# Kernel tuning notes

Measured on AMD Instinct MI355X. Metric: run time of the kernel, lower is better.

The kernel has to match this reference:

```python
import jax, jax.numpy as jnp
import numpy as np

DIM = 1024
HEADS = 16
SCALE = DIM ** (-0.5)  # NOTE: module scales by full dim, not head_dim


def setup_inputs() -> dict:
    key = jax.random.key(0)
    k1, k2, k3, k4 = jax.random.split(key, 4)
    x = jax.random.normal(k1, (4, 2048, DIM), dtype=jnp.float32)
    # torch Linear weights: y = x @ W.T
    w_qkv = jax.random.normal(k2, (3 * DIM, DIM), dtype=jnp.float32) * (DIM ** -0.5)
    w_out = jax.random.normal(k3, (DIM, DIM), dtype=jnp.float32) * (DIM ** -0.5)
    b_out = jax.random.normal(k4, (DIM,), dtype=jnp.float32) * 0.01
    return {"x": x, "w_qkv": w_qkv, "w_out": w_out, "b_out": b_out}


def reference(x, w_qkv, w_out, b_out):
    b, n, _ = x.shape
    h = HEADS
    d = DIM // h
    qkv = x @ w_qkv.T                                   # [b, n, 3*dim]
    qkv = qkv.reshape(b, n, 3, h, d)                    # split (qkv h d)
    qkv = jnp.transpose(qkv, (2, 0, 3, 1, 4))           # [3, b, h, n, d]
    q, k, v = qkv[0], qkv[1], qkv[2]
    dots = jnp.einsum('bhid,bhjd->bhij', q, k) * SCALE  # [b, h, n, n]
    attn = jax.nn.softmax(dots, axis=-1)
    out = jnp.einsum('bhij,bhjd->bhid', attn, v)        # [b, h, n, d]
    out = jnp.transpose(out, (0, 2, 1, 3)).reshape(b, n, h * d)
    return out @ w_out.T + b_out
```

## Files before the change

kernel.cpp:

```cpp
#include <hip/hip_runtime.h>

typedef short bf16x8 __attribute__((ext_vector_type(8)));
typedef _Float16 f16x8 __attribute__((ext_vector_type(8)));
typedef __fp16 fp16x2 __attribute__((ext_vector_type(2)));
typedef float f32x4 __attribute__((ext_vector_type(4)));
typedef float f32x16 __attribute__((ext_vector_type(16)));
typedef unsigned u32x2 __attribute__((ext_vector_type(2)));

static __device__ __forceinline__ unsigned short f2bf(float f) {
  union { float f; unsigned u; } v; v.f = f;
  unsigned r = v.u + 0x7fffu + ((v.u >> 16) & 1u);
  return (unsigned short)(r >> 16);
}

static __device__ __forceinline__ unsigned short f2h(float f) {
  union { _Float16 h; unsigned short u; } c; c.h = (_Float16)f; return c.u;
}

static __device__ __forceinline__ unsigned pkh(float lo, float hi) {
  union { fp16x2 h; unsigned u; } c;
  c.h = __builtin_amdgcn_cvt_pkrtz(lo, hi);
  return c.u;
}

static __device__ __forceinline__ void gll16(const unsigned short* g,
                                             unsigned short* l) {
  __builtin_amdgcn_global_load_lds(
      (const __attribute__((address_space(1))) unsigned int*)g,
      (__attribute__((address_space(3))) unsigned int*)l, 16, 0, 0);
}

__global__ void cvt3_kernel(const float* __restrict__ a,
                            const float* __restrict__ b,
                            const float* __restrict__ c,
                            unsigned short* __restrict__ dst) {
  int i = blockIdx.x * blockDim.x + threadIdx.x;
  const float* src; int off;
  if (i < 2097152) { src = a; off = 0; }
  else if (i < 2883584) { src = b; off = 2097152; }
  else { src = c; off = 2883584; }
  float4 f = ((const float4*)src)[i - off];
  ushort4 o;
  o.x = f2bf(f.x); o.y = f2bf(f.y); o.z = f2bf(f.z); o.w = f2bf(f.w);
  ((ushort4*)dst)[i] = o;
}

#define TM 128
#define TN 128
#define BK 64

template <int EPI>
__global__ __launch_bounds__(256, 3)
void gemm_bt(const unsigned short* __restrict__ X,
             const unsigned short* __restrict__ W,
             unsigned short* __restrict__ QKV, float* __restrict__ OUT,
             const float* __restrict__ bias, int M, int N, int K) {
  __shared__ __align__(16) unsigned short As[TM * BK];
  __shared__ __align__(16) unsigned short Bs[TN * BK];

  const int tid = threadIdx.x;
  const int lane = tid & 63;
  const int wave = tid >> 6;
  const int quad = lane >> 4;
  const int l16 = lane & 15;
  const int wm = wave >> 1, wn = wave & 1;
  const int rc = l16 & 7;

  const int m0 = blockIdx.y * TM;
  const int n0 = blockIdx.x * TN;

  const int sr = lane >> 3;
  const int gsc = ((lane & 7) ^ sr) * 8;

  f32x4 zero = {0.f, 0.f, 0.f, 0.f};
  f32x4 acc[4][4];
#pragma unroll
  for (int i = 0; i < 4; i++)
#pragma unroll
    for (int j = 0; j < 4; j++) acc[i][j] = zero;

  for (int k0 = 0; k0 < K; k0 += BK) {
    __syncthreads();
#pragma unroll
    for (int c = 0; c < 4; c++) {
      int row = wave * 32 + c * 8;
      gll16(&X[(size_t)(m0 + row + sr) * K + k0 + gsc], &As[row * BK]);
      gll16(&W[(size_t)(n0 + row + sr) * K + k0 + gsc], &Bs[row * BK]);
    }
    __syncthreads();
#pragma unroll
    for (int kk = 0; kk < 2; kk++) {
      bf16x8 af[4], bfr[4];
      const int csw = ((kk * 4 + quad) ^ rc) * 8;
#pragma unroll
      for (int t = 0; t < 4; t++) {
        af[t]  = *(const bf16x8*)&As[(wm * 64 + t * 16 + l16) * BK + csw];
        bfr[t] = *(const bf16x8*)&Bs[(wn * 64 + t * 16 + l16) * BK + csw];
      }
#pragma unroll
      for (int mt = 0; mt < 4; mt++)
#pragma unroll
        for (int nt = 0; nt < 4; nt++)
          acc[mt][nt] = __builtin_amdgcn_mfma_f32_16x16x32_bf16(
              af[mt], bfr[nt], acc[mt][nt], 0, 0, 0);
    }
  }

#pragma unroll
  for (int mt = 0; mt < 4; mt++) {
#pragma unroll
    for (int nt = 0; nt < 4; nt++) {
      if (EPI == 0) {
        int nbase = n0 + wn * 64 + nt * 16;
        int which = nbase >> 10;
        if (which == 2) {
          int rem = (nbase + l16) & 1023;
          int h = rem >> 6, dd = rem & 63;
          int growb = m0 + wm * 64 + mt * 16 + quad * 4;
          int b = growb >> 11, nn0 = growb & 2047;
          ushort4 o;
          o.x = f2h(acc[mt][nt][0]);
          o.y = f2h(acc[mt][nt][1]);
          o.z = f2h(acc[mt][nt][2]);
          o.w = f2h(acc[mt][nt][3]);
          *(ushort4*)&QKV[16777216u + (((size_t)(b * 16 + h) * 64 + dd) << 11) + nn0] = o;
        } else {
#pragma unroll
          for (int r = 0; r < 4; r++) {
            int grow = m0 + wm * 64 + mt * 16 + quad * 4 + r;
            int gcol = nbase + l16;
            int rem = gcol & 1023;
            int h = rem >> 6, dd = rem & 63;
            float v = acc[mt][nt][r];
            if (which == 0) v *= 0.04508422f;
            int b = grow >> 11, nn = grow & 2047;
            QKV[(size_t)which * 8388608 +
                ((size_t)(b * 16 + h) * 2048 + nn) * 64 + dd] = f2bf(v);
          }
        }
      } else {
#pragma unroll
        for (int r = 0; r < 4; r++) {
          int grow = m0 + wm * 64 + mt * 16 + quad * 4 + r;
          int gcol = n0 + wn * 64 + nt * 16 + l16;
          OUT[(size_t)grow * N + gcol] = acc[mt][nt][r] + bias[gcol];
        }
      }
    }
  }
}

#define SK 72

__global__ __launch_bounds__(512, 4)
void attn_kernel(const unsigned short* __restrict__ Qg,
                 const unsigned short* __restrict__ Kg,
                 const unsigned short* __restrict__ Vg,
                 unsigned short* __restrict__ AO) {
  __shared__ __align__(16) unsigned short K_s[2][64 * SK];
  __shared__ __align__(16) unsigned short V_s[2][64 * SK];

  const int tid = threadIdx.x;
  const int lane = tid & 63;
  const int wave = tid >> 6;
  const int l31 = lane & 31;
  const int hh = lane >> 5;

  const int id = blockIdx.x + 8 * blockIdx.y;
  const int xcd = id & 7;
  const int slot = id >> 3;
  const int bh = xcd * 8 + (slot & 7);
  const int qb = slot >> 3;

  const size_t base = (size_t)bh * 131072;
  const int q0 = qb * 256 + wave * 32;

  bf16x8 bq[4];
#pragma unroll
  for (int ks = 0; ks < 4; ks++)
    bq[ks] = *(const bf16x8*)&Qg[base + (size_t)(q0 + l31) * 64 + ks * 16 + hh * 8];

  f32x16 O[2];
#pragma unroll
  for (int dt = 0; dt < 2; dt++)
#pragma unroll
    for (int r = 0; r < 16; r++) O[dt][r] = 0.f;
  float lrow = 0.f;

  const int sr = lane >> 3, sc = (lane & 7) * 8;
  const unsigned short* Kp = Kg + base + (size_t)(wave * 8 + sr) * 64 + sc;
  const unsigned short* Vp = Vg + base + (size_t)(wave * 8 + sr) * 2048 + sc;
  const int woff = (wave * 8 + sr) * SK + sc;

  uint4 kr, vr;
  kr = *(const uint4*)Kp;
  vr = *(const uint4*)Vp;
  *(uint4*)&K_s[0][woff] = kr;
  *(uint4*)&V_s[0][woff] = vr;
  __syncthreads();

  for (int t = 0; t < 32; t++) {
    const unsigned short* Kc = K_s[t & 1];
    const unsigned short* Vc = V_s[t & 1];
    if (t < 31) {
      kr = *(const uint4*)(Kp + (size_t)(t + 1) * 4096);
      vr = *(const uint4*)(Vp + (size_t)(t + 1) * 64);
    }

    f32x16 S[2];
#pragma unroll
    for (int sub = 0; sub < 2; sub++) {
      f32x16 a;
#pragma unroll
      for (int r = 0; r < 16; r++) a[r] = 0.f;
#pragma unroll
      for (int ks = 0; ks < 4; ks++) {
        bf16x8 kf = *(const bf16x8*)&Kc[(sub * 32 + l31) * SK + ks * 16 + hh * 8];
        a = __builtin_amdgcn_mfma_f32_32x32x16_bf16(kf, bq[ks], a, 0, 0, 0);
      }
      S[sub] = a;
    }

    float rsum = 0.f;
#pragma unroll
    for (int sub = 0; sub < 2; sub++)
#pragma unroll
      for (int r = 0; r < 16; r++) {
        float p = __builtin_amdgcn_exp2f(S[sub][r]);
        S[sub][r] = p;
        rsum += p;
      }
    lrow += rsum;

#pragma unroll
    for (int win = 0; win < 4; win++) {
      const int sub = win >> 1, kk = win & 1;
      const int g0 = kk * 2, g1 = kk * 2 + 1;
      unsigned a00 = pkh(S[sub][4 * g0 + 0], S[sub][4 * g0 + 1]);
      unsigned a01 = pkh(S[sub][4 * g0 + 2], S[sub][4 * g0 + 3]);
      unsigned a10 = pkh(S[sub][4 * g1 + 0], S[sub][4 * g1 + 1]);
      unsigned a11 = pkh(S[sub][4 * g1 + 2], S[sub][4 * g1 + 3]);
      union { unsigned u[4]; f16x8 v; } fr;
#if __has_builtin(__builtin_amdgcn_permlane32_swap)
      u32x2 r0 = __builtin_amdgcn_permlane32_swap(a00, a10, false, false);
      u32x2 r1 = __builtin_amdgcn_permlane32_swap(a01, a11, false, false);
      fr.u[0] = r0.x; fr.u[1] = r1.x; fr.u[2] = r0.y; fr.u[3] = r1.y;
#else
      unsigned b00 = __shfl_xor((int)a00, 32);
      unsigned b01 = __shfl_xor((int)a01, 32);
      unsigned b10 = __shfl_xor((int)a10, 32);
      unsigned b11 = __shfl_xor((int)a11, 32);
      fr.u[0] = hh ? b10 : a00;
      fr.u[1] = hh ? b11 : a01;
      fr.u[2] = hh ? a10 : b00;
      fr.u[3] = hh ? a11 : b01;
#endif
      f16x8 pf = fr.v;
#pragma unroll
      for (int dt = 0; dt < 2; dt++) {
        f16x8 vf = *(const f16x8*)&Vc[(dt * 32 + l31) * SK + win * 16 + hh * 8];
        O[dt] = __builtin_amdgcn_mfma_f32_32x32x16_f16(vf, pf, O[dt], 0, 0, 0);
      }
    }

    if (t < 31) {
      const int nb = (t + 1) & 1;
      *(uint4*)&K_s[nb][woff] = kr;
      *(uint4*)&V_s[nb][woff] = vr;
    }
    __syncthreads();
  }

  const int b4 = bh >> 4, head = bh & 15;
  lrow += __shfl_xor(lrow, 32);
  float inv = 1.0f / lrow;
  int row = b4 * 2048 + q0 + l31;
#pragma unroll
  for (int dt = 0; dt < 2; dt++)
#pragma unroll
    for (int g = 0; g < 4; g++) {
      ushort4 o;
      o.x = f2bf(O[dt][4 * g + 0] * inv);
      o.y = f2bf(O[dt][4 * g + 1] * inv);
      o.z = f2bf(O[dt][4 * g + 2] * inv);
      o.w = f2bf(O[dt][4 * g + 3] * inv);
      *(ushort4*)&AO[(size_t)row * 1024 + head * 64 + dt * 32 + 8 * g + 4 * hh] = o;
    }
}

extern "C" void kernel_launch(void* const* d_in, const int* in_sizes, int n_in,
                              void* d_out, int out_size, void* d_ws,
                              size_t ws_size, hipStream_t stream) {
  const float* x     = (const float*)d_in[0];
  const float* w_qkv = (const float*)d_in[1];
  const float* w_out = (const float*)d_in[2];
  const float* b_out = (const float*)d_in[3];
  float* out = (float*)d_out;

  unsigned short* ws = (unsigned short*)d_ws;
  unsigned short* Xbf  = ws;
  unsigned short* Wqkv = ws + 8388608;
  unsigned short* Wout = ws + 11534336;
  unsigned short* QKV  = ws + 12582912;
  unsigned short* AO   = ws;

  cvt3_kernel<<<12288, 256, 0, stream>>>(x, w_qkv, w_out, Xbf);

  gemm_bt<0><<<dim3(3072 / TN, 8192 / TM), 256, 0, stream>>>(
      Xbf, Wqkv, QKV, nullptr, nullptr, 8192, 3072, 1024);

  attn_kernel<<<dim3(8, 64), 512, 0, stream>>>(
      QKV, QKV + 8388608, QKV + 16777216, AO);

  gemm_bt<1><<<dim3(1024 / TN, 8192 / TM), 256, 0, stream>>>(
      AO, Wout, nullptr, out, b_out, 8192, 1024, 1024);
}
```

Baseline: 250.0 us.

## Replace QKV projection GEMM with 256x256-tile, 8-wave pipelined kernel

```diff
diff --git a/kernel.cpp b/kernel.cpp
--- a/kernel.cpp
+++ b/kernel.cpp
@@ -45,15 +45,253 @@
   ((ushort4*)dst)[i] = o;
 }
 
+__global__ __launch_bounds__(512, 2)
+void gemm256_qkv(const unsigned short* __restrict__ X,
+                 const unsigned short* __restrict__ W,
+                 unsigned short* __restrict__ QKV, int M, int N, int K) {
+  __shared__ __align__(16) unsigned short As[2][2][256 * 32];
+  __shared__ __align__(16) unsigned short Bs[2][2][256 * 32];
+
+  const int tid = threadIdx.x;
+  const int lane = tid & 63;
+  const int wave = tid >> 6;
+  const int wm = wave >> 2;
+  const int wn = wave & 3;
+  const int quad = lane >> 4;
+  const int l16 = lane & 15;
+
+  const int id = blockIdx.x + 12 * blockIdx.y;
+  const int nid = (id & 7) * 48 + (id >> 3);
+  const int n0 = (nid % 12) * 256;
+  const int m0 = (nid / 12) * 256;
+
+  const int rl = lane >> 2;
+  const int sl = lane & 3;
+  const int gchunk = ((sl ^ (rl & 3)) * 8);
+  const int aslot = (quad ^ (l16 & 3)) * 8;
+
+  auto stageA = [&](int b, int kh, int T) {
+#pragma unroll
+    for (int c = 0; c < 2; c++) {
+      int row = wave * 32 + c * 16;
+      gll16(&X[(size_t)(m0 + row + rl) * K + T * 64 + kh * 32 + gchunk],
+            &As[b][kh][row * 32]);
+    }
+  };
+  auto stageB = [&](int b, int kh, int T) {
+#pragma unroll
+    for (int c = 0; c < 2; c++) {
+      int row = wave * 32 + c * 16;
+      gll16(&W[(size_t)(n0 + row + rl) * K + T * 64 + kh * 32 + gchunk],
+            &Bs[b][kh][row * 32]);
+    }
+  };
+
+  f32x4 zero = {0.f, 0.f, 0.f, 0.f};
+  f32x4 acc[8][4];
+#pragma unroll
+  for (int i = 0; i < 8; i++)
+#pragma unroll
+    for (int j = 0; j < 4; j++) acc[i][j] = zero;
+
+  bf16x8 af[8], bfb[4];
+
+  const int NI = K >> 7;
+
+  stageA(0, 0, 0); stageB(0, 0, 0); stageA(0, 1, 0); stageB(0, 1, 0);
+  stageA(1, 0, 1); stageB(1, 0, 1);
+  asm volatile("s_waitcnt vmcnt(4)" ::: "memory");
+  __builtin_amdgcn_s_barrier();
+
+  for (int i = 0; i < NI; i++) {
+    const int T = 2 * i;
+    const int U = T + 1;
+    const bool more = (i + 1 < NI);
+
+#pragma unroll
+    for (int mt = 0; mt < 8; mt++)
+      af[mt] = *(const bf16x8*)&As[0][0][(wm * 128 + mt * 16 + l16) * 32 + aslot];
+#pragma unroll
+    for (int nt = 0; nt < 2; nt++)
+      bfb[nt] = *(const bf16x8*)&Bs[0][0][(wn * 64 + nt * 16 + l16) * 32 + aslot];
+    stageA(1, 1, U);
+    __builtin_amdgcn_s_barrier();
+    __builtin_amdgcn_s_setprio(1);
+#pragma unroll
+    for (int mt = 0; mt < 8; mt++)
+#pragma unroll
+      for (int nt = 0; nt < 2; nt++)
+        acc[mt][nt] = __builtin_amdgcn_mfma_f32_16x16x32_bf16(
+            af[mt], bfb[nt], acc[mt][nt], 0, 0, 0);
+    __builtin_amdgcn_s_setprio(0);
+    __builtin_amdgcn_s_barrier();
+
+#pragma unroll
+    for (int nt = 0; nt < 2; nt++)
+      bfb[2 + nt] = *(const bf16x8*)&Bs[0][0][(wn * 64 + (2 + nt) * 16 + l16) * 32 + aslot];
+    stageB(1, 1, U);
+    __builtin_amdgcn_s_barrier();
+    __builtin_amdgcn_s_setprio(1);
+#pragma unroll
+    for (int mt = 0; mt < 8; mt++)
+#pragma unroll
+      for (int nt = 0; nt < 2; nt++)
+        acc[mt][2 + nt] = __builtin_amdgcn_mfma_f32_16x16x32_bf16(
+            af[mt], bfb[2 + nt], acc[mt][2 + nt], 0, 0, 0);
+    __builtin_amdgcn_s_setprio(0);
+    __builtin_amdgcn_s_barrier();
+
+#pragma unroll
+    for (int mt = 0; mt < 8; mt++)
+      af[mt] = *(const bf16x8*)&As[0][1][(wm * 128 + mt * 16 + l16) * 32 + aslot];
+#pragma unroll
+    for (int nt = 0; nt < 2; nt++)
+      bfb[nt] = *(const bf16x8*)&Bs[0][1][(wn * 64 + nt * 16 + l16) * 32 + aslot];
+    if (more) stageA(0, 0, T + 2);
+    __builtin_amdgcn_s_barrier();
+    __builtin_amdgcn_s_setprio(1);
+#pragma unroll
+    for (int mt = 0; mt < 8; mt++)
+#pragma unroll
+      for (int nt = 0; nt < 2; nt++)
+        acc[mt][nt] = __builtin_amdgcn_mfma_f32_16x16x32_bf16(
+            af[mt], bfb[nt], acc[mt][nt], 0, 0, 0);
+    __builtin_amdgcn_s_setprio(0);
+    __builtin_amdgcn_s_barrier();
+
+#pragma unroll
+    for (int nt = 0; nt < 2; nt++)
+      bfb[2 + nt] = *(const bf16x8*)&Bs[0][1][(wn * 64 + (2 + nt) * 16 + l16) * 32 + aslot];
+    if (more) {
+      stageB(0, 0, T + 2);
+      asm volatile("s_waitcnt vmcnt(4)" ::: "memory");
+    } else {
+      asm volatile("s_waitcnt vmcnt(0)" ::: "memory");
+    }
+    __builtin_amdgcn_s_barrier();
+    __builtin_amdgcn_s_setprio(1);
+#pragma unroll
+    for (int mt = 0; mt < 8; mt++)
+#pragma unroll
+      for (int nt = 0; nt < 2; nt++)
+        acc[mt][2 + nt] = __builtin_amdgcn_mfma_f32_16x16x32_bf16(
+            af[mt], bfb[2 + nt], acc[mt][2 + nt], 0, 0, 0);
+    __builtin_amdgcn_s_setprio(0);
+    __builtin_amdgcn_s_barrier();
+
+#pragma unroll
+    for (int mt = 0; mt < 8; mt++)
+      af[mt] = *(const bf16x8*)&As[1][0][(wm * 128 + mt * 16 + l16) * 32 + aslot];
+#pragma unroll
+    for (int nt = 0; nt < 2; nt++)
+      bfb[nt] = *(const bf16x8*)&Bs[1][0][(wn * 64 + nt * 16 + l16) * 32 + aslot];
+    if (more) stageA(0, 1, T + 2);
+    __builtin_amdgcn_s_barrier();
+    __builtin_amdgcn_s_setprio(1);
+#pragma unroll
+    for (int mt = 0; mt < 8; mt++)
+#pragma unroll
+      for (int nt = 0; nt < 2; nt++)
+        acc[mt][nt] = __builtin_amdgcn_mfma_f32_16x16x32_bf16(
+            af[mt], bfb[nt], acc[mt][nt], 0, 0, 0);
+    __builtin_amdgcn_s_setprio(0);
+    __builtin_amdgcn_s_barrier();
+
+#pragma unroll
+    for (int nt = 0; nt < 2; nt++)
+      bfb[2 + nt] = *(const bf16x8*)&Bs[1][0][(wn * 64 + (2 + nt) * 16 + l16) * 32 + aslot];
+    if (more) stageB(0, 1, T + 2);
+    __builtin_amdgcn_s_barrier();
+    __builtin_amdgcn_s_setprio(1);
+#pragma unroll
+    for (int mt = 0; mt < 8; mt++)
+#pragma unroll
+      for (int nt = 0; nt < 2; nt++)
+        acc[mt][2 + nt] = __builtin_amdgcn_mfma_f32_16x16x32_bf16(
+            af[mt], bfb[2 + nt], acc[mt][2 + nt], 0, 0, 0);
+    __builtin_amdgcn_s_setprio(0);
+    __builtin_amdgcn_s_barrier();
+
+#pragma unroll
+    for (int mt = 0; mt < 8; mt++)
+      af[mt] = *(const bf16x8*)&As[1][1][(wm * 128 + mt * 16 + l16) * 32 + aslot];
+#pragma unroll
+    for (int nt = 0; nt < 2; nt++)
+      bfb[nt] = *(const bf16x8*)&Bs[1][1][(wn * 64 + nt * 16 + l16) * 32 + aslot];
+    if (more) stageA(1, 0, U + 2);
+    __builtin_amdgcn_s_barrier();
+    __builtin_amdgcn_s_setprio(1);
+#pragma unroll
+    for (int mt = 0; mt < 8; mt++)
+#pragma unroll
+      for (int nt = 0; nt < 2; nt++)
+        acc[mt][nt] = __builtin_amdgcn_mfma_f32_16x16x32_bf16(
+            af[mt], bfb[nt], acc[mt][nt], 0, 0, 0);
+    __builtin_amdgcn_s_setprio(0);
+    __builtin_amdgcn_s_barrier();
+
+#pragma unroll
+    for (int nt = 0; nt < 2; nt++)
+      bfb[2 + nt] = *(const bf16x8*)&Bs[1][1][(wn * 64 + (2 + nt) * 16 + l16) * 32 + aslot];
+    if (more) {
+      stageB(1, 0, U + 2);
+      asm volatile("s_waitcnt vmcnt(4)" ::: "memory");
+    }
+    __builtin_amdgcn_s_barrier();
+    __builtin_amdgcn_s_setprio(1);
+#pragma unroll
+    for (int mt = 0; mt < 8; mt++)
+#pragma unroll
+      for (int nt = 0; nt < 2; nt++)
+        acc[mt][2 + nt] = __builtin_amdgcn_mfma_f32_16x16x32_bf16(
+            af[mt], bfb[2 + nt], acc[mt][2 + nt], 0, 0, 0);
+    __builtin_amdgcn_s_setprio(0);
+    __builtin_amdgcn_s_barrier();
+  }
+
+#pragma unroll
+  for (int mt = 0; mt < 8; mt++) {
+#pragma unroll
+    for (int nt = 0; nt < 4; nt++) {
+      int nbase = n0 + wn * 64 + nt * 16;
+      int which = nbase >> 10;
+      if (which == 2) {
+        int rem = (nbase + l16) & 1023;
+        int h = rem >> 6, dd = rem & 63;
+        int growb = m0 + wm * 128 + mt * 16 + quad * 4;
+        int b = growb >> 11, nn0 = growb & 2047;
+        ushort4 o;
+        o.x = f2h(acc[mt][nt][0]);
+        o.y = f2h(acc[mt][nt][1]);
+        o.z = f2h(acc[mt][nt][2]);
+        o.w = f2h(acc[mt][nt][3]);
+        *(ushort4*)&QKV[16777216u + (((size_t)(b * 16 + h) * 64 + dd) << 11) + nn0] = o;
+      } else {
+#pragma unroll
+        for (int r = 0; r < 4; r++) {
+          int grow = m0 + wm * 128 + mt * 16 + quad * 4 + r;
+          int gcol = nbase + l16;
+          int rem = gcol & 1023;
+          int h = rem >> 6, dd = rem & 63;
+          float v = acc[mt][nt][r];
+          if (which == 0) v *= 0.04508422f;
+          int b = grow >> 11, nn = grow & 2047;
+          QKV[(size_t)which * 8388608 +
+              ((size_t)(b * 16 + h) * 2048 + nn) * 64 + dd] = f2bf(v);
+        }
+      }
+    }
+  }
+}
+
 #define TM 128
 #define TN 128
 #define BK 64
 
-template <int EPI>
 __global__ __launch_bounds__(256, 3)
 void gemm_bt(const unsigned short* __restrict__ X,
              const unsigned short* __restrict__ W,
-             unsigned short* __restrict__ QKV, float* __restrict__ OUT,
+             float* __restrict__ OUT,
              const float* __restrict__ bias, int M, int N, int K) {
   __shared__ __align__(16) unsigned short As[TM * BK];
   __shared__ __align__(16) unsigned short Bs[TN * BK];
@@ -110,41 +348,11 @@
   for (int mt = 0; mt < 4; mt++) {
 #pragma unroll
     for (int nt = 0; nt < 4; nt++) {
-      if (EPI == 0) {
-        int nbase = n0 + wn * 64 + nt * 16;
-        int which = nbase >> 10;
-        if (which == 2) {
-          int rem = (nbase + l16) & 1023;
-          int h = rem >> 6, dd = rem & 63;
-          int growb = m0 + wm * 64 + mt * 16 + quad * 4;
-          int b = growb >> 11, nn0 = growb & 2047;
-          ushort4 o;
-          o.x = f2h(acc[mt][nt][0]);
-          o.y = f2h(acc[mt][nt][1]);
-          o.z = f2h(acc[mt][nt][2]);
-          o.w = f2h(acc[mt][nt][3]);
-          *(ushort4*)&QKV[16777216u + (((size_t)(b * 16 + h) * 64 + dd) << 11) + nn0] = o;
-        } else {
-#pragma unroll
-          for (int r = 0; r < 4; r++) {
-            int grow = m0 + wm * 64 + mt * 16 + quad * 4 + r;
-            int gcol = nbase + l16;
-            int rem = gcol & 1023;
-            int h = rem >> 6, dd = rem & 63;
-            float v = acc[mt][nt][r];
-            if (which == 0) v *= 0.04508422f;
-            int b = grow >> 11, nn = grow & 2047;
-            QKV[(size_t)which * 8388608 +
-                ((size_t)(b * 16 + h) * 2048 + nn) * 64 + dd] = f2bf(v);
-          }
-        }
-      } else {
-#pragma unroll
-        for (int r = 0; r < 4; r++) {
-          int grow = m0 + wm * 64 + mt * 16 + quad * 4 + r;
-          int gcol = n0 + wn * 64 + nt * 16 + l16;
-          OUT[(size_t)grow * N + gcol] = acc[mt][nt][r] + bias[gcol];
-        }
+#pragma unroll
+      for (int r = 0; r < 4; r++) {
+        int grow = m0 + wm * 64 + mt * 16 + quad * 4 + r;
+        int gcol = n0 + wn * 64 + nt * 16 + l16;
+        OUT[(size_t)grow * N + gcol] = acc[mt][nt][r] + bias[gcol];
       }
     }
   }
@@ -306,12 +514,12 @@
 
   cvt3_kernel<<<12288, 256, 0, stream>>>(x, w_qkv, w_out, Xbf);
 
-  gemm_bt<0><<<dim3(3072 / TN, 8192 / TM), 256, 0, stream>>>(
-      Xbf, Wqkv, QKV, nullptr, nullptr, 8192, 3072, 1024);
+  gemm256_qkv<<<dim3(12, 32), 512, 0, stream>>>(
+      Xbf, Wqkv, QKV, 8192, 3072, 1024);
 
   attn_kernel<<<dim3(8, 64), 512, 0, stream>>>(
       QKV, QKV + 8388608, QKV + 16777216, AO);
 
-  gemm_bt<1><<<dim3(1024 / TN, 8192 / TM), 256, 0, stream>>>(
-      AO, Wout, nullptr, out, b_out, 8192, 1024, 1024);
-}
+  gemm_bt<<<dim3(1024 / TN, 8192 / TM), 256, 0, stream>>>(
+      AO, Wout, out, b_out, 8192, 1024, 1024);
+}
```

After: 267.2 us. +6.9%, slower.

## Replace QKV projection GEMM with 256x256 tiled, software-pipelined 8-wave kernel

Applied to the files above, without the earlier changes.

```diff
diff --git a/kernel.cpp b/kernel.cpp
--- a/kernel.cpp
+++ b/kernel.cpp
@@ -45,15 +45,193 @@
   ((ushort4*)dst)[i] = o;
 }
 
+__global__ __launch_bounds__(512, 2)
+void gemm256_qkv(const unsigned short* __restrict__ X,
+                 const unsigned short* __restrict__ W,
+                 unsigned short* __restrict__ QKV, int M, int N, int K) {
+  __shared__ __align__(16) unsigned short As[2][2][128 * 64];
+  __shared__ __align__(16) unsigned short Bs[2][2][128 * 64];
+
+  const int tid = threadIdx.x;
+  const int lane = tid & 63;
+  const int wave = tid >> 6;
+  const int wm = wave >> 2;
+  const int wn = wave & 3;
+  const int quad = lane >> 4;
+  const int l16 = lane & 15;
+  const int l8 = l16 & 7;
+
+  const int id = blockIdx.x + 12 * blockIdx.y;
+  const int nid = (id & 7) * 48 + (id >> 3);
+  const int n0 = (nid % 12) * 256;
+  const int m0 = (nid / 12) * 256;
+
+  const int sr8 = lane >> 3;
+  const int gsc = ((lane & 7) ^ sr8) * 8;
+
+  auto stA = [&](int b, int mh, int T) {
+#pragma unroll
+    for (int c = 0; c < 2; c++) {
+      int row = wave * 16 + c * 8;
+      gll16(&X[(size_t)(m0 + mh * 128 + row + sr8) * K + T * 64 + gsc],
+            &As[b][mh][row * 64]);
+    }
+  };
+  auto stB = [&](int b, int nh, int T) {
+#pragma unroll
+    for (int c = 0; c < 2; c++) {
+      int row = wave * 16 + c * 8;
+      gll16(&W[(size_t)(n0 + nh * 128 + row + sr8) * K + T * 64 + gsc],
+            &Bs[b][nh][row * 64]);
+    }
+  };
+
+  f32x4 zero = {0.f, 0.f, 0.f, 0.f};
+  f32x4 acc[8][4];
+#pragma unroll
+  for (int i = 0; i < 8; i++)
+#pragma unroll
+    for (int j = 0; j < 4; j++) acc[i][j] = zero;
+
+  bf16x8 af[4][2], bf[2][2];
+
+  auto ldA = [&](int b, int mh) {
+#pragma unroll
+    for (int m = 0; m < 4; m++)
+#pragma unroll
+      for (int kk = 0; kk < 2; kk++)
+        af[m][kk] = *(const bf16x8*)&As[b][mh][(wm * 64 + m * 16 + l16) * 64 +
+                                               ((kk * 4 + quad) ^ l8) * 8];
+  };
+  auto ldB = [&](int b, int nh) {
+#pragma unroll
+    for (int n = 0; n < 2; n++)
+#pragma unroll
+      for (int kk = 0; kk < 2; kk++)
+        bf[n][kk] = *(const bf16x8*)&Bs[b][nh][(wn * 32 + n * 16 + l16) * 64 +
+                                               ((kk * 4 + quad) ^ l8) * 8];
+  };
+
+  auto MFMA16 = [&](int mb, int nb) {
+    __builtin_amdgcn_s_setprio(1);
+#pragma unroll
+    for (int kk = 0; kk < 2; kk++)
+#pragma unroll
+      for (int m = 0; m < 4; m++)
+#pragma unroll
+        for (int n = 0; n < 2; n++)
+          acc[mb + m][nb + n] = __builtin_amdgcn_mfma_f32_16x16x32_bf16(
+              af[m][kk], bf[n][kk], acc[mb + m][nb + n], 0, 0, 0);
+    __builtin_amdgcn_s_setprio(0);
+  };
+
+  const int NI = K >> 7;
+
+  stA(0, 0, 0); stB(0, 0, 0); stA(0, 1, 0); stB(0, 1, 0);
+  stA(1, 0, 1); stB(1, 1, 1);
+  asm volatile("s_waitcnt vmcnt(4)" ::: "memory");
+  __builtin_amdgcn_s_barrier();
+
+  for (int i = 0; i < NI; i++) {
+    const int T = 2 * i;
+    const int U = T + 1;
+    const bool more = (i + 1 < NI);
+
+    ldA(0, 0); ldB(0, 0);
+    stA(1, 1, U);
+    __builtin_amdgcn_s_barrier();
+    MFMA16(0, 0);
+    __builtin_amdgcn_s_barrier();
+
+    ldB(0, 1);
+    stB(1, 0, U);
+    __builtin_amdgcn_s_barrier();
+    MFMA16(0, 2);
+    __builtin_amdgcn_s_barrier();
+
+    ldA(0, 1);
+    if (more) stA(0, 0, T + 2);
+    __builtin_amdgcn_s_barrier();
+    MFMA16(4, 2);
+    __builtin_amdgcn_s_barrier();
+
+    ldB(0, 0);
+    if (more) stB(0, 1, T + 2);
+    __builtin_amdgcn_s_barrier();
+    MFMA16(4, 0);
+    if (more) asm volatile("s_waitcnt vmcnt(4)" ::: "memory");
+    else      asm volatile("s_waitcnt vmcnt(0)" ::: "memory");
+    __builtin_amdgcn_s_barrier();
+
+    ldA(1, 0); ldB(1, 0);
+    if (more) stA(0, 1, T + 2);
+    __builtin_amdgcn_s_barrier();
+    MFMA16(0, 0);
+    __builtin_amdgcn_s_barrier();
+
+    ldB(1, 1);
+    if (more) stB(0, 0, T + 2);
+    __builtin_amdgcn_s_barrier();
+    MFMA16(0, 2);
+    __builtin_amdgcn_s_barrier();
+
+    ldA(1, 1);
+    if (more) stA(1, 0, T + 3);
+    __builtin_amdgcn_s_barrier();
+    MFMA16(4, 2);
+    __builtin_amdgcn_s_barrier();
+
+    ldB(1, 0);
+    if (more) stB(1, 1, T + 3);
+    __builtin_amdgcn_s_barrier();
+    MFMA16(4, 0);
+    if (more) asm volatile("s_waitcnt vmcnt(4)" ::: "memory");
+    __builtin_amdgcn_s_barrier();
+  }
+
+#pragma unroll
+  for (int mt = 0; mt < 8; mt++) {
+    const int growb = m0 + (mt >> 2) * 128 + wm * 64 + (mt & 3) * 16 + quad * 4;
+#pragma unroll
+    for (int nt = 0; nt < 4; nt++) {
+      int nbase = n0 + (nt >> 1) * 128 + wn * 32 + (nt & 1) * 16;
+      int which = nbase >> 10;
+      if (which == 2) {
+        int rem = (nbase + l16) & 1023;
+        int h = rem >> 6, dd = rem & 63;
+        int b = growb >> 11, nn0 = growb & 2047;
+        ushort4 o;
+        o.x = f2h(acc[mt][nt][0]);
+        o.y = f2h(acc[mt][nt][1]);
+        o.z = f2h(acc[mt][nt][2]);
+        o.w = f2h(acc[mt][nt][3]);
+        *(ushort4*)&QKV[16777216u + (((size_t)(b * 16 + h) * 64 + dd) << 11) + nn0] = o;
+      } else {
+#pragma unroll
+        for (int r = 0; r < 4; r++) {
+          int grow = growb + r;
+          int gcol = nbase + l16;
+          int rem = gcol & 1023;
+          int h = rem >> 6, dd = rem & 63;
+          float v = acc[mt][nt][r];
+          if (which == 0) v *= 0.04508422f;
+          int b = grow >> 11, nn = grow & 2047;
+          QKV[(size_t)which * 8388608 +
+              ((size_t)(b * 16 + h) * 2048 + nn) * 64 + dd] = f2bf(v);
+        }
+      }
+    }
+  }
+}
+
 #define TM 128
 #define TN 128
 #define BK 64
 
-template <int EPI>
 __global__ __launch_bounds__(256, 3)
 void gemm_bt(const unsigned short* __restrict__ X,
              const unsigned short* __restrict__ W,
-             unsigned short* __restrict__ QKV, float* __restrict__ OUT,
+             float* __restrict__ OUT,
              const float* __restrict__ bias, int M, int N, int K) {
   __shared__ __align__(16) unsigned short As[TM * BK];
   __shared__ __align__(16) unsigned short Bs[TN * BK];
@@ -110,41 +288,11 @@
   for (int mt = 0; mt < 4; mt++) {
 #pragma unroll
     for (int nt = 0; nt < 4; nt++) {
-      if (EPI == 0) {
-        int nbase = n0 + wn * 64 + nt * 16;
-        int which = nbase >> 10;
-        if (which == 2) {
-          int rem = (nbase + l16) & 1023;
-          int h = rem >> 6, dd = rem & 63;
-          int growb = m0 + wm * 64 + mt * 16 + quad * 4;
-          int b = growb >> 11, nn0 = growb & 2047;
-          ushort4 o;
-          o.x = f2h(acc[mt][nt][0]);
-          o.y = f2h(acc[mt][nt][1]);
-          o.z = f2h(acc[mt][nt][2]);
-          o.w = f2h(acc[mt][nt][3]);
-          *(ushort4*)&QKV[16777216u + (((size_t)(b * 16 + h) * 64 + dd) << 11) + nn0] = o;
-        } else {
-#pragma unroll
-          for (int r = 0; r < 4; r++) {
-            int grow = m0 + wm * 64 + mt * 16 + quad * 4 + r;
-            int gcol = nbase + l16;
-            int rem = gcol & 1023;
-            int h = rem >> 6, dd = rem & 63;
-            float v = acc[mt][nt][r];
-            if (which == 0) v *= 0.04508422f;
-            int b = grow >> 11, nn = grow & 2047;
-            QKV[(size_t)which * 8388608 +
-                ((size_t)(b * 16 + h) * 2048 + nn) * 64 + dd] = f2bf(v);
-          }
-        }
-      } else {
-#pragma unroll
-        for (int r = 0; r < 4; r++) {
-          int grow = m0 + wm * 64 + mt * 16 + quad * 4 + r;
-          int gcol = n0 + wn * 64 + nt * 16 + l16;
-          OUT[(size_t)grow * N + gcol] = acc[mt][nt][r] + bias[gcol];
-        }
+#pragma unroll
+      for (int r = 0; r < 4; r++) {
+        int grow = m0 + wm * 64 + mt * 16 + quad * 4 + r;
+        int gcol = n0 + wn * 64 + nt * 16 + l16;
+        OUT[(size_t)grow * N + gcol] = acc[mt][nt][r] + bias[gcol];
       }
     }
   }
@@ -306,12 +454,12 @@
 
   cvt3_kernel<<<12288, 256, 0, stream>>>(x, w_qkv, w_out, Xbf);
 
-  gemm_bt<0><<<dim3(3072 / TN, 8192 / TM), 256, 0, stream>>>(
-      Xbf, Wqkv, QKV, nullptr, nullptr, 8192, 3072, 1024);
+  gemm256_qkv<<<dim3(12, 32), 512, 0, stream>>>(
+      Xbf, Wqkv, QKV, 8192, 3072, 1024);
 
   attn_kernel<<<dim3(8, 64), 512, 0, stream>>>(
       QKV, QKV + 8388608, QKV + 16777216, AO);
 
-  gemm_bt<1><<<dim3(1024 / TN, 8192 / TM), 256, 0, stream>>>(
-      AO, Wout, nullptr, out, b_out, 8192, 1024, 1024);
-}
+  gemm_bt<<<dim3(1024 / TN, 8192 / TM), 256, 0, stream>>>(
+      AO, Wout, out, b_out, 8192, 1024, 1024);
+}
```

Measured after the change: 275.7 us. 10.3% more time.
